# Kernel tuning notes

Measured on AMD Instinct MI355X. Metric: run time of the kernel, lower is better.

## Reference

```python
import jax, jax.numpy as jnp
import numpy as np
import math

B, T, E = 2, 2048, 2048
G, QPG, D = 4, 4, 128  # kv groups, queries per group, head dim (G*QPG*D == E)


def sinusoidal_pe(t, d, dtype):
    pos = jnp.arange(t, dtype=jnp.float32)[:, None]            # [T,1]
    i = jnp.arange(0, d, 2, dtype=jnp.float32)                 # [D/2]
    inv_freq = jnp.exp(-(jnp.log(10000.0) * i / d))            # [D/2]
    ang = pos * inv_freq                                       # [T,D/2]
    pe = jnp.zeros((t, d), dtype=jnp.float32)
    pe = pe.at[:, 0::2].set(jnp.sin(ang)).at[:, 1::2].set(jnp.cos(ang))
    return pe.astype(dtype)


def setup_inputs() -> dict:
    key = jax.random.key(0)
    ks = jax.random.split(key, 6)
    s = lambda fan_in: 1.0 / math.sqrt(fan_in)
    return {
        "x":   jax.random.normal(ks[0], (B, T, E), dtype=jnp.float32),
        "wq":  jax.random.uniform(ks[1], (E, G * QPG * D), jnp.float32, -s(E), s(E)),
        "bq":  jax.random.uniform(ks[2], (G * QPG * D,), jnp.float32, -s(E), s(E)),
        "wkv": jax.random.uniform(ks[3], (E, 2 * G * D), jnp.float32, -s(E), s(E)),
        "bkv": jax.random.uniform(ks[4], (2 * G * D,), jnp.float32, -s(E), s(E)),
        "wo":  jax.random.uniform(ks[5], (G * QPG * D, E), jnp.float32, -s(G * QPG * D), s(G * QPG * D)),
    }


def reference(x, wq, bq, wkv, bkv, wo):
    b, t, e = x.shape
    # projections
    q = (x @ wq + bq).reshape(b, t, G, QPG, D).transpose(0, 2, 3, 1, 4)   # [B,G,QPG,T,D]
    kv = (x @ wkv + bkv).reshape(b, t, G, 1, 2 * D).transpose(0, 2, 3, 1, 4)  # [B,G,1,T,2D]
    k, v = kv[..., :D], kv[..., D:]                                       # [B,G,1,T,D]
    # inline additive sinusoidal positional embedding on q and k
    pe = sinusoidal_pe(t, D, x.dtype)                                     # [T,D]
    q = q + pe
    k = k + pe
    # scores: [B,G,QPG,T,T] (kv head axis k has size 1, summed out)
    scores = jnp.einsum('bgqtd,bgksd->bgqts', q, k) / math.sqrt(D)
    causal = jnp.tril(jnp.ones((t, t), dtype=bool))                       # [T,T]
    scores = jnp.where(causal, scores, -jnp.inf)
    probs = jax.nn.softmax(scores, axis=-1)
    out = jnp.einsum('bgqts,bgksd->btgqd', probs, v).reshape(b, t, G * QPG * D)
    return out @ wo
```

## Files before the change

### kernel.cpp

```cpp
#include <hip/hip_runtime.h>
#include <stdint.h>

typedef __bf16 bf16;
typedef __bf16 bf16x4 __attribute__((ext_vector_type(4)));
typedef __bf16 bf16x8 __attribute__((ext_vector_type(8)));
typedef float floatx4 __attribute__((ext_vector_type(4)));

#define B_   2
#define T_   2048
#define E_   2048
#define G_   4
#define QPG_ 4
#define D_   128
#define H_   16
#define NQ   2048
#define NKV  1024
#define NQKV 3072
#define M_   4096

__device__ __forceinline__ void gload_lds16(const void* g, void* l) {
  __builtin_amdgcn_global_load_lds(
      (__attribute__((address_space(1))) unsigned int*)g,
      (__attribute__((address_space(3))) unsigned int*)l,
      16, 0, 0);
}

__device__ __forceinline__ int swz_stage_col(int lane) {
  return (((lane & 3) ^ ((lane >> 2) & 3) ^ ((lane >> 4) & 3))) * 8;
}


__global__ void cast_f32_bf16(const float* __restrict__ in, bf16* __restrict__ out, int n4) {
  int i = blockIdx.x * blockDim.x + threadIdx.x;
  if (i < n4) {
    float4 v = ((const float4*)in)[i];
    bf16x4 o = {(bf16)v.x, (bf16)v.y, (bf16)v.z, (bf16)v.w};
    ((bf16x4*)out)[i] = o;
  }
}

__global__ void transpose_cast(const float* __restrict__ in, bf16* __restrict__ out,
                               int R, int C, int out_stride) {
  __shared__ float tile[64][65];
  int r0 = blockIdx.x * 64, c0 = blockIdx.y * 64;
  int tx = threadIdx.x & 63, ty = threadIdx.x >> 6;
  for (int i = ty; i < 64; i += 4)
    tile[i][tx] = in[(size_t)(r0 + i) * C + c0 + tx];
  __syncthreads();
  for (int i = ty; i < 64; i += 4)
    out[(size_t)(c0 + i) * out_stride + r0 + tx] = (bf16)tile[tx][i];
}

__global__ void concat_bias(const float* __restrict__ bq, const float* __restrict__ bkv,
                            float* __restrict__ out) {
  int i = blockIdx.x * 256 + threadIdx.x;
  out[i] = (i < NQ) ? bq[i] : bkv[i - NQ];
}


template <int OUT_BF16, int HAS_BIAS>
__global__ __launch_bounds__(256, 2) void gemm_bt(
    const bf16* __restrict__ A, const bf16* __restrict__ Bt,
    const float* __restrict__ bias, void* __restrict__ Cout,
    int M, int N, int K) {
  __shared__ __align__(16) bf16 As[128 * 32];
  __shared__ __align__(16) bf16 Bs[128 * 32];
  const int tid = threadIdx.x;
  const int wave = tid >> 6, lane = tid & 63;
  const int quad = lane >> 4, c = lane & 15;
  const int m0 = blockIdx.x * 128, n0 = blockIdx.y * 128;
  const int wr = (wave >> 1) * 64, wc = (wave & 1) * 64;
  const int xsl = ((quad ^ (c & 3) ^ ((c >> 2) & 3)) & 3) * 8;

  floatx4 acc[4][4];
#pragma unroll
  for (int i = 0; i < 4; ++i)
#pragma unroll
    for (int j = 0; j < 4; ++j) acc[i][j] = (floatx4){0.f, 0.f, 0.f, 0.f};

  const int srow = wave * 32 + (lane >> 2);
  const int scol = swz_stage_col(lane);
  const bf16* Ap = A + (size_t)(m0 + srow) * K + scol;
  const bf16* Bp = Bt + (size_t)(n0 + srow) * K + scol;

  for (int k0 = 0; k0 < K; k0 += 32) {
#pragma unroll
    for (int ch = 0; ch < 2; ++ch) {
      gload_lds16(Ap + (size_t)ch * 16 * K + k0, &As[(wave * 2 + ch) * 512]);
      gload_lds16(Bp + (size_t)ch * 16 * K + k0, &Bs[(wave * 2 + ch) * 512]);
    }
    __syncthreads();
    bf16x8 af[4], bfr[4];
#pragma unroll
    for (int i = 0; i < 4; ++i) {
      af[i]  = *(const bf16x8*)(&As[(wr + i * 16 + c) * 32 + xsl]);
      bfr[i] = *(const bf16x8*)(&Bs[(wc + i * 16 + c) * 32 + xsl]);
    }
#pragma unroll
    for (int mi = 0; mi < 4; ++mi)
#pragma unroll
      for (int ni = 0; ni < 4; ++ni)
        acc[mi][ni] = __builtin_amdgcn_mfma_f32_16x16x32_bf16(af[mi], bfr[ni], acc[mi][ni], 0, 0, 0);
    __syncthreads();
  }

  float bv[4] = {0.f, 0.f, 0.f, 0.f};
  if (HAS_BIAS) {
#pragma unroll
    for (int ni = 0; ni < 4; ++ni) bv[ni] = bias[n0 + wc + ni * 16 + c];
  }
#pragma unroll
  for (int mi = 0; mi < 4; ++mi) {
#pragma unroll
    for (int ni = 0; ni < 4; ++ni) {
      const int col = n0 + wc + ni * 16 + c;
#pragma unroll
      for (int r = 0; r < 4; ++r) {
        const int row = m0 + wr + mi * 16 + quad * 4 + r;
        float v = acc[mi][ni][r] + bv[ni];
        if (OUT_BF16)
          ((bf16*)Cout)[(size_t)row * N + col] = (bf16)v;
        else
          ((float*)Cout)[(size_t)row * N + col] = v;
      }
    }
  }
}


__device__ __forceinline__ float pe_val(int t, int d) {
  int i2 = d & ~1;
  float inv = __expf(-9.210340371976184f * (float)i2 * (1.0f / 128.0f));
  float ang = (float)t * inv;
  return (d & 1) ? cosf(ang) : sinf(ang);
}

__global__ void scatter_qk(const bf16* __restrict__ qkv,
                           bf16* __restrict__ Qb, bf16* __restrict__ Kb) {
  const int row = blockIdx.x;
  const int b = row >> 11, t = row & 2047;
  const int tid = threadIdx.x;
  const int d = tid & 127;
  const float scale = 0.12751745f;
  const float pe = pe_val(t, d);
  for (int h = tid >> 7; h < H_; h += 2) {
    float q = (float)qkv[(size_t)row * NQKV + h * 128 + d] + pe;
    Qb[((size_t)(b * H_ + h) * T_ + t) * D_ + d] = (bf16)(q * scale);
  }
  for (int g = tid >> 7; g < G_; g += 2) {
    float k = (float)qkv[(size_t)row * NQKV + NQ + g * 256 + d] + pe;
    Kb[((size_t)(b * G_ + g) * T_ + t) * D_ + d] = (bf16)k;
  }
}

__global__ void build_vt(const bf16* __restrict__ qkv, bf16* __restrict__ Vt) {
  __shared__ float tile[64][65];
  int t0 = blockIdx.x * 64, d0 = blockIdx.y * 64;
  int bg = blockIdx.z, b = bg >> 2, g = bg & 3;
  const bf16* src = qkv + (size_t)b * T_ * NQKV + NQ + g * 256 + 128;
  bf16* dst = Vt + (size_t)bg * D_ * T_;
  int tx = threadIdx.x & 63, ty = threadIdx.x >> 6;
  for (int i = ty; i < 64; i += 4)
    tile[i][tx] = (float)src[(size_t)(t0 + i) * NQKV + d0 + tx];
  __syncthreads();
  for (int i = ty; i < 64; i += 4)
    dst[(size_t)(d0 + i) * T_ + t0 + tx] = (bf16)tile[tx][i];
}


__global__ __launch_bounds__(256, 4) void flash_attn(
    const bf16* __restrict__ Qb, const bf16* __restrict__ Kb,
    const bf16* __restrict__ Vt, bf16* __restrict__ Ob) {
  const int qt = (blockIdx.x + blockIdx.y) & 31;
  const int bh = blockIdx.y;
  const int b = bh >> 4, h = bh & 15, g = h >> 2;
  const int tid = threadIdx.x;
  const int wave = tid >> 6, lane = tid & 63;
  const int quad = lane >> 4, c = lane & 15;
  const int xsl = ((quad ^ (c & 3) ^ ((c >> 2) & 3)) & 3) * 8;

  __shared__ __align__(16) bf16 Ks[2][4][32 * 32];
  __shared__ __align__(16) bf16 Vs[2][4][32 * 32];
  __shared__ __align__(16) bf16 Pq[4][16 * 40];

  const int q0 = qt * 64;
  const bf16* Qbase = Qb + ((size_t)(b * H_ + h) * T_ + q0 + wave * 16 + c) * D_;
  bf16x8 qf[4];
#pragma unroll
  for (int ks = 0; ks < 4; ++ks)
    qf[ks] = *(const bf16x8*)(Qbase + ks * 32 + quad * 8);

  floatx4 acc[8];
#pragma unroll
  for (int i = 0; i < 8; ++i) acc[i] = (floatx4){0.f, 0.f, 0.f, 0.f};
  float rsum[4] = {0.f, 0.f, 0.f, 0.f};

  const bf16* Kg = Kb + (size_t)(b * G_ + g) * T_ * D_;
  const bf16* Vg = Vt + (size_t)(b * G_ + g) * D_ * T_;
  const int slr = lane >> 2;
  const int slc = swz_stage_col(lane);
  const int nt = 2 * qt + 2;

  auto stage = [&](int t, int bu) {
    const int k0 = t * 32;
#pragma unroll
    for (int hh = 0; hh < 2; ++hh)
      gload_lds16(Kg + (size_t)(k0 + hh * 16 + slr) * D_ + wave * 32 + slc,
                  &Ks[bu][wave][hh * 16 * 32]);
#pragma unroll
    for (int hh = 0; hh < 2; ++hh)
      gload_lds16(Vg + (size_t)(wave * 32 + hh * 16 + slr) * T_ + k0 + slc,
                  &Vs[bu][wave][hh * 16 * 32]);
  };

  stage(0, 0);

  for (int j = 0; j < nt; ++j) {
    __syncthreads();
    if (j + 1 < nt) stage(j + 1, (j + 1) & 1);

    const bf16* Kt  = &Ks[j & 1][0][0];
    const bf16* Vtl = &Vs[j & 1][0][0];

    floatx4 s[2];
    s[0] = (floatx4){0.f, 0.f, 0.f, 0.f};
    s[1] = (floatx4){0.f, 0.f, 0.f, 0.f};
#pragma unroll
    for (int ks = 0; ks < 4; ++ks)
#pragma unroll
      for (int n = 0; n < 2; ++n) {
        bf16x8 kf = *(const bf16x8*)(Kt + ks * 1024 + (n * 16 + c) * 32 + xsl);
        s[n] = __builtin_amdgcn_mfma_f32_16x16x32_bf16(qf[ks], kf, s[n], 0, 0, 0);
      }

    if (j >= 2 * qt) {
      const int colb = j * 32;
      const int rowb = q0 + wave * 16 + quad * 4;
#pragma unroll
      for (int n = 0; n < 2; ++n)
#pragma unroll
        for (int r = 0; r < 4; ++r)
          if (colb + n * 16 + c > rowb + r) s[n][r] = -1e30f;
    }

    float pvv[2][4];
#pragma unroll
    for (int n = 0; n < 2; ++n)
#pragma unroll
      for (int r = 0; r < 4; ++r) {
        float p = exp2f(s[n][r]);
        pvv[n][r] = p;
        rsum[r] += p;
      }

    bf16* Pw = &Pq[wave][0];
#pragma unroll
    for (int n = 0; n < 2; ++n)
#pragma unroll
      for (int r = 0; r < 4; ++r)
        Pw[(quad * 4 + r) * 40 + n * 16 + c] = (bf16)pvv[n][r];

    bf16x8 pf = *(const bf16x8*)(&Pw[c * 40 + quad * 8]);

#pragma unroll
    for (int nd = 0; nd < 8; ++nd) {
      bf16x8 vf = *(const bf16x8*)(Vtl + (nd >> 1) * 1024 + ((nd & 1) * 16 + c) * 32 + xsl);
      acc[nd] = __builtin_amdgcn_mfma_f32_16x16x32_bf16(pf, vf, acc[nd], 0, 0, 0);
    }
  }

#pragma unroll
  for (int off = 1; off < 16; off <<= 1)
#pragma unroll
    for (int r = 0; r < 4; ++r) rsum[r] += __shfl_xor(rsum[r], off);

  float linv[4];
#pragma unroll
  for (int r = 0; r < 4; ++r) linv[r] = 1.f / rsum[r];
#pragma unroll
  for (int nd = 0; nd < 8; ++nd) {
    const int dd = nd * 16 + c;
#pragma unroll
    for (int r = 0; r < 4; ++r) {
      const int trow = q0 + wave * 16 + quad * 4 + r;
      Ob[((size_t)(b * T_ + trow)) * NQ + h * D_ + dd] = (bf16)(acc[nd][r] * linv[r]);
    }
  }
}


extern "C" void kernel_launch(void* const* d_in, const int* in_sizes, int n_in,
                              void* d_out, int out_size, void* d_ws, size_t ws_size,
                              hipStream_t stream) {
  const float* x   = (const float*)d_in[0];
  const float* wq  = (const float*)d_in[1];
  const float* bq  = (const float*)d_in[2];
  const float* wkv = (const float*)d_in[3];
  const float* bkv = (const float*)d_in[4];
  const float* wo  = (const float*)d_in[5];
  float* out = (float*)d_out;

  char* p = (char*)d_ws;
  bf16* xb    = (bf16*)p; p += (size_t)M_ * E_ * 2;
  bf16* wqkvT = (bf16*)p; p += (size_t)NQKV * E_ * 2;
  bf16* woT   = (bf16*)p; p += (size_t)E_ * NQ * 2;
  float* biasq = (float*)p; p += 16384;
  bf16* qkv   = (bf16*)p; p += (size_t)M_ * NQKV * 2;
  bf16* Qb    = (bf16*)p; p += (size_t)B_ * H_ * T_ * D_ * 2;
  bf16* Kb    = (bf16*)p; p += (size_t)B_ * G_ * T_ * D_ * 2;
  bf16* Vtb   = (bf16*)p; p += (size_t)B_ * G_ * D_ * T_ * 2;
  bf16* Ob    = (bf16*)p; p += (size_t)M_ * NQ * 2;

  cast_f32_bf16<<<(M_ * E_ / 4) / 256, 256, 0, stream>>>(x, xb, M_ * E_ / 4);
  transpose_cast<<<dim3(E_ / 64, E_ / 64), 256, 0, stream>>>(wq, wqkvT, E_, E_, E_);
  transpose_cast<<<dim3(E_ / 64, NKV / 64), 256, 0, stream>>>(wkv, wqkvT + (size_t)NQ * E_, E_, NKV, E_);
  transpose_cast<<<dim3(E_ / 64, E_ / 64), 256, 0, stream>>>(wo, woT, NQ, E_, NQ);
  concat_bias<<<NQKV / 256, 256, 0, stream>>>(bq, bkv, biasq);

  gemm_bt<1, 1><<<dim3(M_ / 128, NQKV / 128), 256, 0, stream>>>(xb, wqkvT, biasq, qkv, M_, NQKV, E_);
  scatter_qk<<<M_, 256, 0, stream>>>(qkv, Qb, Kb);
  build_vt<<<dim3(T_ / 64, D_ / 64, B_ * G_), 256, 0, stream>>>(qkv, Vtb);
  flash_attn<<<dim3(T_ / 64, B_ * H_), 256, 0, stream>>>(Qb, Kb, Vtb, Ob);
  gemm_bt<0, 0><<<dim3(M_ / 128, E_ / 128), 256, 0, stream>>>(Ob, woT, nullptr, out, M_, E_, NQ);
}
```

Measured before the change: 332.0 us.

## Fuse QKV scatter/PE/V-transpose into GEMM epilogue; two query tiles per attention wave

The QKV projection GEMM now writes Q (with positional embedding and scale), K (with PE) and transposed V directly from its epilogue. This removes the intermediate qkv buffer and the separate scatter and transpose kernels, and a small kernel precomputes the PE table. The flash attention kernel drops to 128 threads with each wave handling 32 query rows, reusing each K/V fragment across two MFMAs. The risks are uncoalesced strided stores for the V transpose in the GEMM epilogue and fewer waves per block for latency hiding.

Measured after the change: 338.2 us. About the same (+1.8%).

```diff
diff --git a/kernel.cpp b/kernel.cpp
--- a/kernel.cpp
+++ b/kernel.cpp
@@ -57,12 +57,18 @@
   out[i] = (i < NQ) ? bq[i] : bkv[i - NQ];
 }
 
-
-template <int OUT_BF16, int HAS_BIAS>
+__global__ void build_pe(float* __restrict__ pe) {
+  const int t = blockIdx.x, d = threadIdx.x;
+  const int i2 = d & ~1;
+  float inv = expf(-9.210340371976184f * (float)i2 * (1.0f / 128.0f));
+  float ang = (float)t * inv;
+  pe[t * 128 + d] = (d & 1) ? cosf(ang) : sinf(ang);
+}
+
+
 __global__ __launch_bounds__(256, 2) void gemm_bt(
     const bf16* __restrict__ A, const bf16* __restrict__ Bt,
-    const float* __restrict__ bias, void* __restrict__ Cout,
-    int M, int N, int K) {
+    float* __restrict__ Cout, int M, int N, int K) {
   __shared__ __align__(16) bf16 As[128 * 32];
   __shared__ __align__(16) bf16 Bs[128 * 32];
   const int tid = threadIdx.x;
@@ -104,71 +110,98 @@
     __syncthreads();
   }
 
-  float bv[4] = {0.f, 0.f, 0.f, 0.f};
-  if (HAS_BIAS) {
-#pragma unroll
-    for (int ni = 0; ni < 4; ++ni) bv[ni] = bias[n0 + wc + ni * 16 + c];
-  }
-#pragma unroll
-  for (int mi = 0; mi < 4; ++mi) {
+#pragma unroll
+  for (int mi = 0; mi < 4; ++mi)
 #pragma unroll
     for (int ni = 0; ni < 4; ++ni) {
       const int col = n0 + wc + ni * 16 + c;
 #pragma unroll
       for (int r = 0; r < 4; ++r) {
         const int row = m0 + wr + mi * 16 + quad * 4 + r;
-        float v = acc[mi][ni][r] + bv[ni];
-        if (OUT_BF16)
-          ((bf16*)Cout)[(size_t)row * N + col] = (bf16)v;
-        else
-          ((float*)Cout)[(size_t)row * N + col] = v;
-      }
-    }
-  }
-}
-
-
-__device__ __forceinline__ float pe_val(int t, int d) {
-  int i2 = d & ~1;
-  float inv = __expf(-9.210340371976184f * (float)i2 * (1.0f / 128.0f));
-  float ang = (float)t * inv;
-  return (d & 1) ? cosf(ang) : sinf(ang);
-}
-
-__global__ void scatter_qk(const bf16* __restrict__ qkv,
-                           bf16* __restrict__ Qb, bf16* __restrict__ Kb) {
-  const int row = blockIdx.x;
-  const int b = row >> 11, t = row & 2047;
+        Cout[(size_t)row * N + col] = acc[mi][ni][r];
+      }
+    }
+}
+
+
+__global__ __launch_bounds__(256, 2) void gemm_qkv(
+    const bf16* __restrict__ A, const bf16* __restrict__ Bt,
+    const float* __restrict__ bias, const float* __restrict__ peT,
+    bf16* __restrict__ Qb, bf16* __restrict__ Kb, bf16* __restrict__ Vtb) {
+  const int N = NQKV, K = E_;
+  __shared__ __align__(16) bf16 As[128 * 32];
+  __shared__ __align__(16) bf16 Bs[128 * 32];
   const int tid = threadIdx.x;
-  const int d = tid & 127;
+  const int wave = tid >> 6, lane = tid & 63;
+  const int quad = lane >> 4, c = lane & 15;
+  const int m0 = blockIdx.x * 128, n0 = blockIdx.y * 128;
+  const int wr = (wave >> 1) * 64, wc = (wave & 1) * 64;
+  const int xsl = ((quad ^ (c & 3) ^ ((c >> 2) & 3)) & 3) * 8;
+
+  floatx4 acc[4][4];
+#pragma unroll
+  for (int i = 0; i < 4; ++i)
+#pragma unroll
+    for (int j = 0; j < 4; ++j) acc[i][j] = (floatx4){0.f, 0.f, 0.f, 0.f};
+
+  const int srow = wave * 32 + (lane >> 2);
+  const int scol = swz_stage_col(lane);
+  const bf16* Ap = A + (size_t)(m0 + srow) * K + scol;
+  const bf16* Bp = Bt + (size_t)(n0 + srow) * K + scol;
+
+  for (int k0 = 0; k0 < K; k0 += 32) {
+#pragma unroll
+    for (int ch = 0; ch < 2; ++ch) {
+      gload_lds16(Ap + (size_t)ch * 16 * K + k0, &As[(wave * 2 + ch) * 512]);
+      gload_lds16(Bp + (size_t)ch * 16 * K + k0, &Bs[(wave * 2 + ch) * 512]);
+    }
+    __syncthreads();
+    bf16x8 af[4], bfr[4];
+#pragma unroll
+    for (int i = 0; i < 4; ++i) {
+      af[i]  = *(const bf16x8*)(&As[(wr + i * 16 + c) * 32 + xsl]);
+      bfr[i] = *(const bf16x8*)(&Bs[(wc + i * 16 + c) * 32 + xsl]);
+    }
+#pragma unroll
+    for (int mi = 0; mi < 4; ++mi)
+#pragma unroll
+      for (int ni = 0; ni < 4; ++ni)
+        acc[mi][ni] = __builtin_amdgcn_mfma_f32_16x16x32_bf16(af[mi], bfr[ni], acc[mi][ni], 0, 0, 0);
+    __syncthreads();
+  }
+
   const float scale = 0.12751745f;
-  const float pe = pe_val(t, d);
-  for (int h = tid >> 7; h < H_; h += 2) {
-    float q = (float)qkv[(size_t)row * NQKV + h * 128 + d] + pe;
-    Qb[((size_t)(b * H_ + h) * T_ + t) * D_ + d] = (bf16)(q * scale);
-  }
-  for (int g = tid >> 7; g < G_; g += 2) {
-    float k = (float)qkv[(size_t)row * NQKV + NQ + g * 256 + d] + pe;
-    Kb[((size_t)(b * G_ + g) * T_ + t) * D_ + d] = (bf16)k;
-  }
-}
-
-__global__ void build_vt(const bf16* __restrict__ qkv, bf16* __restrict__ Vt) {
-  __shared__ float tile[64][65];
-  int t0 = blockIdx.x * 64, d0 = blockIdx.y * 64;
-  int bg = blockIdx.z, b = bg >> 2, g = bg & 3;
-  const bf16* src = qkv + (size_t)b * T_ * NQKV + NQ + g * 256 + 128;
-  bf16* dst = Vt + (size_t)bg * D_ * T_;
-  int tx = threadIdx.x & 63, ty = threadIdx.x >> 6;
-  for (int i = ty; i < 64; i += 4)
-    tile[i][tx] = (float)src[(size_t)(t0 + i) * NQKV + d0 + tx];
-  __syncthreads();
-  for (int i = ty; i < 64; i += 4)
-    dst[(size_t)(d0 + i) * T_ + t0 + tx] = (bf16)tile[tx][i];
-}
-
-
-__global__ __launch_bounds__(256, 4) void flash_attn(
+#pragma unroll
+  for (int ni = 0; ni < 4; ++ni) {
+    const int col = n0 + wc + ni * 16 + c;
+    const float bv = bias[col];
+#pragma unroll
+    for (int mi = 0; mi < 4; ++mi) {
+#pragma unroll
+      for (int r = 0; r < 4; ++r) {
+        const int row = m0 + wr + mi * 16 + quad * 4 + r;
+        const int bb = row >> 11, t = row & 2047;
+        float v = acc[mi][ni][r] + bv;
+        if (col < NQ) {
+          const int h = col >> 7, d = col & 127;
+          Qb[((size_t)(bb * H_ + h) * T_ + t) * D_ + d] =
+              (bf16)((v + peT[t * 128 + d]) * scale);
+        } else {
+          const int cc = col - NQ, g = cc >> 8, w2 = cc & 255;
+          if (w2 < 128) {
+            Kb[((size_t)(bb * G_ + g) * T_ + t) * D_ + w2] =
+                (bf16)(v + peT[t * 128 + w2]);
+          } else {
+            Vtb[((size_t)(bb * G_ + g) * D_ + (w2 - 128)) * T_ + t] = (bf16)v;
+          }
+        }
+      }
+    }
+  }
+}
+
+
+__global__ __launch_bounds__(128, 2) void flash_attn(
     const bf16* __restrict__ Qb, const bf16* __restrict__ Kb,
     const bf16* __restrict__ Vt, bf16* __restrict__ Ob) {
   const int qt = (blockIdx.x + blockIdx.y) & 31;
@@ -181,19 +214,24 @@
 
   __shared__ __align__(16) bf16 Ks[2][4][32 * 32];
   __shared__ __align__(16) bf16 Vs[2][4][32 * 32];
-  __shared__ __align__(16) bf16 Pq[4][16 * 40];
+  __shared__ __align__(16) bf16 Pq[2][32 * 40];
 
   const int q0 = qt * 64;
-  const bf16* Qbase = Qb + ((size_t)(b * H_ + h) * T_ + q0 + wave * 16 + c) * D_;
-  bf16x8 qf[4];
-#pragma unroll
-  for (int ks = 0; ks < 4; ++ks)
-    qf[ks] = *(const bf16x8*)(Qbase + ks * 32 + quad * 8);
-
-  floatx4 acc[8];
-#pragma unroll
-  for (int i = 0; i < 8; ++i) acc[i] = (floatx4){0.f, 0.f, 0.f, 0.f};
-  float rsum[4] = {0.f, 0.f, 0.f, 0.f};
+  const int qw = q0 + wave * 32;
+  const bf16* Qh = Qb + (size_t)(b * H_ + h) * T_ * D_;
+  bf16x8 qf[2][4];
+#pragma unroll
+  for (int mi = 0; mi < 2; ++mi)
+#pragma unroll
+    for (int ks = 0; ks < 4; ++ks)
+      qf[mi][ks] = *(const bf16x8*)(Qh + (size_t)(qw + mi * 16 + c) * D_ + ks * 32 + quad * 8);
+
+  floatx4 acc[2][8];
+#pragma unroll
+  for (int mi = 0; mi < 2; ++mi)
+#pragma unroll
+    for (int i = 0; i < 8; ++i) acc[mi][i] = (floatx4){0.f, 0.f, 0.f, 0.f};
+  float rsum[2][4] = {{0.f, 0.f, 0.f, 0.f}, {0.f, 0.f, 0.f, 0.f}};
 
   const bf16* Kg = Kb + (size_t)(b * G_ + g) * T_ * D_;
   const bf16* Vg = Vt + (size_t)(b * G_ + g) * D_ * T_;
@@ -204,13 +242,17 @@
   auto stage = [&](int t, int bu) {
     const int k0 = t * 32;
 #pragma unroll
-    for (int hh = 0; hh < 2; ++hh)
-      gload_lds16(Kg + (size_t)(k0 + hh * 16 + slr) * D_ + wave * 32 + slc,
-                  &Ks[bu][wave][hh * 16 * 32]);
-#pragma unroll
-    for (int hh = 0; hh < 2; ++hh)
-      gload_lds16(Vg + (size_t)(wave * 32 + hh * 16 + slr) * T_ + k0 + slc,
-                  &Vs[bu][wave][hh * 16 * 32]);
+    for (int cc = 0; cc < 2; ++cc) {
+      const int ch = wave * 2 + cc;
+#pragma unroll
+      for (int hh = 0; hh < 2; ++hh)
+        gload_lds16(Kg + (size_t)(k0 + hh * 16 + slr) * D_ + ch * 32 + slc,
+                    &Ks[bu][ch][hh * 16 * 32]);
+#pragma unroll
+      for (int hh = 0; hh < 2; ++hh)
+        gload_lds16(Vg + (size_t)(ch * 32 + hh * 16 + slr) * T_ + k0 + slc,
+                    &Vs[bu][ch][hh * 16 * 32]);
+    }
   };
 
   stage(0, 0);
@@ -222,68 +264,80 @@
     const bf16* Kt  = &Ks[j & 1][0][0];
     const bf16* Vtl = &Vs[j & 1][0][0];
 
-    floatx4 s[2];
-    s[0] = (floatx4){0.f, 0.f, 0.f, 0.f};
-    s[1] = (floatx4){0.f, 0.f, 0.f, 0.f};
+    floatx4 s[2][2];
+#pragma unroll
+    for (int mi = 0; mi < 2; ++mi)
+#pragma unroll
+      for (int n = 0; n < 2; ++n) s[mi][n] = (floatx4){0.f, 0.f, 0.f, 0.f};
 #pragma unroll
     for (int ks = 0; ks < 4; ++ks)
 #pragma unroll
       for (int n = 0; n < 2; ++n) {
         bf16x8 kf = *(const bf16x8*)(Kt + ks * 1024 + (n * 16 + c) * 32 + xsl);
-        s[n] = __builtin_amdgcn_mfma_f32_16x16x32_bf16(qf[ks], kf, s[n], 0, 0, 0);
-      }
-
-    if (j >= 2 * qt) {
-      const int colb = j * 32;
-      const int rowb = q0 + wave * 16 + quad * 4;
+#pragma unroll
+        for (int mi = 0; mi < 2; ++mi)
+          s[mi][n] = __builtin_amdgcn_mfma_f32_16x16x32_bf16(qf[mi][ks], kf, s[mi][n], 0, 0, 0);
+      }
+
+    const int colb = j * 32;
+#pragma unroll
+    for (int mi = 0; mi < 2; ++mi) {
+      if (colb + 31 > qw + mi * 16) {
+        const int rowb = qw + mi * 16 + quad * 4;
+#pragma unroll
+        for (int n = 0; n < 2; ++n)
+#pragma unroll
+          for (int r = 0; r < 4; ++r)
+            if (colb + n * 16 + c > rowb + r) s[mi][n][r] = -1e30f;
+      }
+    }
+
+    bf16* Pw = &Pq[wave][0];
+#pragma unroll
+    for (int mi = 0; mi < 2; ++mi)
 #pragma unroll
       for (int n = 0; n < 2; ++n)
 #pragma unroll
-        for (int r = 0; r < 4; ++r)
-          if (colb + n * 16 + c > rowb + r) s[n][r] = -1e30f;
-    }
-
-    float pvv[2][4];
-#pragma unroll
-    for (int n = 0; n < 2; ++n)
-#pragma unroll
-      for (int r = 0; r < 4; ++r) {
-        float p = exp2f(s[n][r]);
-        pvv[n][r] = p;
-        rsum[r] += p;
-      }
-
-    bf16* Pw = &Pq[wave][0];
-#pragma unroll
-    for (int n = 0; n < 2; ++n)
-#pragma unroll
-      for (int r = 0; r < 4; ++r)
-        Pw[(quad * 4 + r) * 40 + n * 16 + c] = (bf16)pvv[n][r];
-
-    bf16x8 pf = *(const bf16x8*)(&Pw[c * 40 + quad * 8]);
+        for (int r = 0; r < 4; ++r) {
+          float p = exp2f(s[mi][n][r]);
+          rsum[mi][r] += p;
+          Pw[(mi * 16 + quad * 4 + r) * 40 + n * 16 + c] = (bf16)p;
+        }
+
+    bf16x8 pf[2];
+#pragma unroll
+    for (int mi = 0; mi < 2; ++mi)
+      pf[mi] = *(const bf16x8*)(&Pw[(mi * 16 + c) * 40 + quad * 8]);
 
 #pragma unroll
     for (int nd = 0; nd < 8; ++nd) {
       bf16x8 vf = *(const bf16x8*)(Vtl + (nd >> 1) * 1024 + ((nd & 1) * 16 + c) * 32 + xsl);
-      acc[nd] = __builtin_amdgcn_mfma_f32_16x16x32_bf16(pf, vf, acc[nd], 0, 0, 0);
+#pragma unroll
+      for (int mi = 0; mi < 2; ++mi)
+        acc[mi][nd] = __builtin_amdgcn_mfma_f32_16x16x32_bf16(pf[mi], vf, acc[mi][nd], 0, 0, 0);
     }
   }
 
 #pragma unroll
   for (int off = 1; off < 16; off <<= 1)
 #pragma unroll
-    for (int r = 0; r < 4; ++r) rsum[r] += __shfl_xor(rsum[r], off);
-
-  float linv[4];
-#pragma unroll
-  for (int r = 0; r < 4; ++r) linv[r] = 1.f / rsum[r];
-#pragma unroll
-  for (int nd = 0; nd < 8; ++nd) {
-    const int dd = nd * 16 + c;
-#pragma unroll
-    for (int r = 0; r < 4; ++r) {
-      const int trow = q0 + wave * 16 + quad * 4 + r;
-      Ob[((size_t)(b * T_ + trow)) * NQ + h * D_ + dd] = (bf16)(acc[nd][r] * linv[r]);
+    for (int mi = 0; mi < 2; ++mi)
+#pragma unroll
+      for (int r = 0; r < 4; ++r) rsum[mi][r] += __shfl_xor(rsum[mi][r], off);
+
+#pragma unroll
+  for (int mi = 0; mi < 2; ++mi) {
+    float linv[4];
+#pragma unroll
+    for (int r = 0; r < 4; ++r) linv[r] = 1.f / rsum[mi][r];
+#pragma unroll
+    for (int nd = 0; nd < 8; ++nd) {
+      const int dd = nd * 16 + c;
+#pragma unroll
+      for (int r = 0; r < 4; ++r) {
+        const int trow = qw + mi * 16 + quad * 4 + r;
+        Ob[((size_t)(b * T_ + trow)) * NQ + h * D_ + dd] = (bf16)(acc[mi][nd][r] * linv[r]);
+      }
     }
   }
 }
@@ -305,7 +359,7 @@
   bf16* wqkvT = (bf16*)p; p += (size_t)NQKV * E_ * 2;
   bf16* woT   = (bf16*)p; p += (size_t)E_ * NQ * 2;
   float* biasq = (float*)p; p += 16384;
-  bf16* qkv   = (bf16*)p; p += (size_t)M_ * NQKV * 2;
+  float* peT  = (float*)p; p += (size_t)T_ * D_ * 4;
   bf16* Qb    = (bf16*)p; p += (size_t)B_ * H_ * T_ * D_ * 2;
   bf16* Kb    = (bf16*)p; p += (size_t)B_ * G_ * T_ * D_ * 2;
   bf16* Vtb   = (bf16*)p; p += (size_t)B_ * G_ * D_ * T_ * 2;
@@ -316,10 +370,9 @@
   transpose_cast<<<dim3(E_ / 64, NKV / 64), 256, 0, stream>>>(wkv, wqkvT + (size_t)NQ * E_, E_, NKV, E_);
   transpose_cast<<<dim3(E_ / 64, E_ / 64), 256, 0, stream>>>(wo, woT, NQ, E_, NQ);
   concat_bias<<<NQKV / 256, 256, 0, stream>>>(bq, bkv, biasq);
-
-  gemm_bt<1, 1><<<dim3(M_ / 128, NQKV / 128), 256, 0, stream>>>(xb, wqkvT, biasq, qkv, M_, NQKV, E_);
-  scatter_qk<<<M_, 256, 0, stream>>>(qkv, Qb, Kb);
-  build_vt<<<dim3(T_ / 64, D_ / 64, B_ * G_), 256, 0, stream>>>(qkv, Vtb);
-  flash_attn<<<dim3(T_ / 64, B_ * H_), 256, 0, stream>>>(Qb, Kb, Vtb, Ob);
-  gemm_bt<0, 0><<<dim3(M_ / 128, E_ / 128), 256, 0, stream>>>(Ob, woT, nullptr, out, M_, E_, NQ);
-}
+  build_pe<<<T_, 128, 0, stream>>>(peT);
+
+  gemm_qkv<<<dim3(M_ / 128, NQKV / 128), 256, 0, stream>>>(xb, wqkvT, biasq, peT, Qb, Kb, Vtb);
+  flash_attn<<<dim3(T_ / 64, B_ * H_), 128, 0, stream>>>(Qb, Kb, Vtb, Ob);
+  gemm_bt<<<dim3(M_ / 128, E_ / 128), 256, 0, stream>>>(Ob, woT, out, M_, E_, NQ);
+}
```
